# Performance work log

Measured on AMD Instinct MI355X. Metric: run time of the kernel, lower is better.

## Reference

```python
import jax, jax.numpy as jnp
import numpy as np


def setup_inputs() -> dict:
    key = jax.random.key(0)
    ks = jax.random.split(key, 13)
    B, T, I, H = 64, 512, 512, 1024
    s_in = 1.0 / np.sqrt(I)
    s_h = 1.0 / np.sqrt(H)
    d = {"x": jax.random.normal(ks[0], (B, T, I), jnp.float32)}
    names_U = ["U_i", "U_f", "U_c", "U_o"]
    names_V = ["V_i", "V_f", "V_c", "V_o"]
    names_b = ["b_i", "b_f", "b_c", "b_o"]
    for j in range(4):
        d[names_U[j]] = jax.random.normal(ks[1 + j], (I, H), jnp.float32) * s_in
        d[names_V[j]] = jax.random.normal(ks[5 + j], (H, H), jnp.float32) * s_h
        d[names_b[j]] = jax.random.normal(ks[9 + j], (H,), jnp.float32) * 0.01
    return d


def _lstm(x, U_i, V_i, b_i, U_f, V_f, b_f, U_c, V_c, b_c, U_o, V_o, b_o):
    B, T, I = x.shape
    H = U_i.shape[1]
    # Precompute input projections for all gates across time: [T, B, 4H]
    U = jnp.concatenate([U_i, U_f, U_c, U_o], axis=1)      # [I, 4H]
    V = jnp.concatenate([V_i, V_f, V_c, V_o], axis=1)      # [H, 4H]
    b = jnp.concatenate([b_i, b_f, b_c, b_o], axis=0)      # [4H]
    xU = jnp.einsum('bti,ig->tbg', x, U) + b               # [T, B, 4H]

    h0 = jnp.zeros((B, H), x.dtype)
    c0 = jnp.zeros((B, H), x.dtype)

    def step(carry, xu_t):
        h, c = carry
        gates = xu_t + h @ V                               # [B, 4H]
        i_t = jax.nn.sigmoid(gates[:, 0 * H:1 * H])
        f_t = jax.nn.sigmoid(gates[:, 1 * H:2 * H])
        g_t = jnp.tanh(gates[:, 2 * H:3 * H])
        o_t = jax.nn.sigmoid(gates[:, 3 * H:4 * H])
        c_new = f_t * c + i_t * g_t
        h_new = o_t * jnp.tanh(c_new)
        return (h_new, c_new), h_new

    (h_T, c_T), hs = jax.lax.scan(step, (h0, c0), xU)      # hs: [T, B, H]
    hidden_seq = jnp.transpose(hs, (1, 0, 2))              # [B, T, H]
    return hidden_seq, h_T, c_T


def reference(x, U_i, V_i, b_i, U_f, V_f, b_f, U_c, V_c, b_c, U_o, V_o, b_o):
    return _lstm(x, U_i, V_i, b_i, U_f, V_f, b_f, U_c, V_c, b_c, U_o, V_o, b_o)
```

## Files before the change

kernel.cpp:

```cpp
#include <hip/hip_runtime.h>

typedef __attribute__((ext_vector_type(8))) _Float16 f16x8;
typedef __attribute__((ext_vector_type(4))) _Float16 f16x4;
typedef __attribute__((ext_vector_type(4))) float f32x4;

#define B_SZ 64
#define T_SZ 512
#define I_SZ 512
#define H_SZ 1024
#define G4   4096
#define NBLK 256

__global__ void trans_kernel(const float* __restrict__ src, _Float16* __restrict__ dst,
                             int R, int q) {
  __shared__ float tile[64][65];
  const int n0 = blockIdx.x * 64;
  const int r0 = blockIdx.y * 64;
  const int x = threadIdx.x & 63, y = threadIdx.x >> 6;
  #pragma unroll
  for (int it = 0; it < 16; ++it) {
    int r = y * 16 + it;
    tile[r][x] = src[(size_t)(r0 + r) * H_SZ + n0 + x];
  }
  __syncthreads();
  #pragma unroll
  for (int it = 0; it < 16; ++it) {
    int rn = y * 16 + it;
    dst[(size_t)(4 * (n0 + rn) + q) * R + r0 + x] = (_Float16)tile[x][rn];
  }
}

__global__ void bias_kernel(const float* __restrict__ b0, const float* __restrict__ b1,
                            const float* __restrict__ b2, const float* __restrict__ b3,
                            float* __restrict__ dst) {
  int g = blockIdx.x * blockDim.x + threadIdx.x;
  if (g >= G4) return;
  int q = g & 3, n = g >> 2;
  const float* s = (q == 0) ? b0 : (q == 1) ? b1 : (q == 2) ? b2 : b3;
  dst[g] = s[n];
}

__device__ __forceinline__ unsigned short f2h(float f) {
  union { unsigned short s; _Float16 h; } c; c.h = (_Float16)f; return c.s;
}

__device__ __forceinline__ void x_issue(const float* x, int b0, int tid, int t, f32x4* xst) {
  #pragma unroll
  for (int j = 0; j < 8; ++j) {
    const int byteoff = j * 4096 + tid * 16;
    const int row  = byteoff >> 11;
    const int colb = byteoff & 2047;
    const char* sp = (const char*)x + (((size_t)(b0 + row) * T_SZ + t) * I_SZ) * 4 + colb;
    asm volatile("global_load_dwordx4 %0, %1, off" : "=v"(xst[j]) : "v"(sp) : "memory");
  }
}
__device__ __forceinline__ void x_write(char* xl, int tid, const f32x4* xst) {
  #pragma unroll
  for (int j = 0; j < 8; ++j) {
    const int byteoff = j * 4096 + tid * 16;
    const int row  = byteoff >> 11;
    const int colb = (byteoff & 2047) >> 1;
    f16x4 v = { (_Float16)xst[j].x, (_Float16)xst[j].y,
                (_Float16)xst[j].z, (_Float16)xst[j].w };
    *(f16x4*)(xl + (row << 10) + (colb ^ ((row & 7) << 4))) = v;
  }
}

__global__ __launch_bounds__(256, 1) void lstm_recur(
    const float* __restrict__ x,
    const _Float16* __restrict__ Ubt,
    const _Float16* __restrict__ Vt,
    const float* __restrict__ biasw,
    float* __restrict__ out,
    _Float16* __restrict__ hbuf,
    unsigned* __restrict__ bar)
{
  __shared__ __align__(16) char hsh[32768];
  __shared__ __align__(16) char xlds[32768];

  const int tid  = threadIdx.x;
  const int wv   = tid >> 6;
  const int lane = tid & 63;
  const int lc   = lane & 15;
  const int lk   = lane >> 4;
  const int blk  = blockIdx.x;
  const int bgrp = blk & 3;
  const int hgrp = blk >> 2;
  const int col0 = hgrp * 64 + wv * 16;
  const int b0   = bgrp * 16;
  const int sw   = (lc & 7) << 4;

  unsigned* flags = bar + bgrp * 256;

  f16x8 bU[16];
  f16x8 bV[32];
  {
    const _Float16* up = Ubt + (size_t)(col0 + lc) * I_SZ + lk * 8;
    #pragma unroll
    for (int ks = 0; ks < 16; ++ks) bU[ks] = *(const f16x8*)(up + ks * 32);
    const _Float16* vp = Vt + (size_t)(col0 + lc) * H_SZ + lk * 8;
    #pragma unroll
    for (int ks = 0; ks < 32; ++ks) bV[ks] = *(const f16x8*)(vp + ks * 32);
  }
  #pragma unroll
  for (int ks = 0; ks < 16; ++ks) asm volatile("" : "+v"(bU[ks]));
  #pragma unroll
  for (int ks = 0; ks < 32; ++ks) asm volatile("" : "+v"(bV[ks]));

  const f32x4 bias4 = *(const f32x4*)(biasw + col0 + lk * 4);
  const int n_gl = hgrp * 16 + wv * 4 + lk;
  const int brow = b0 + lc;
  const size_t HO = (size_t)B_SZ * T_SZ * H_SZ;
  const size_t CO = HO + (size_t)B_SZ * H_SZ;

  float cst = 0.f;

  const int grow = tid >> 4;
  const int gkb  = (tid & 15) * 16;
  const int gsw  = (grow & 7) << 4;

  f32x4 xst[8];
  x_issue(x, b0, tid, 0, xst);
  asm volatile("s_waitcnt vmcnt(0)" ::: "memory");
  __builtin_amdgcn_sched_barrier(0);
  x_write(xlds, tid, xst);
  asm volatile("s_waitcnt lgkmcnt(0)" ::: "memory");
  __builtin_amdgcn_s_barrier();
  __builtin_amdgcn_sched_barrier(0);

#define XPROJ(ks) { \
    const f16x8 a_ = *(const f16x8*)(xl_cur + (lc << 10) + ((((ks) * 64) + lk * 16) ^ sw)); \
    acc[(ks) & 3] = __builtin_amdgcn_mfma_f32_16x16x32_f16(bU[(ks)], a_, acc[(ks) & 3], 0, 0, 0); }
#define HPROJ(ks) { \
    const f16x8 hv = *(const f16x8*)(hsh + (lc << 11) + (((lk * 16) + (ks) * 64) ^ sw)); \
    acc[(ks) & 3] = __builtin_amdgcn_mfma_f32_16x16x32_f16(bV[(ks)], hv, acc[(ks) & 3], 0, 0, 0); }

  for (int t = 0; t < T_SZ; ++t) {
    const _Float16* hcur  = hbuf + (size_t)(t & 1) * (B_SZ * H_SZ);
    _Float16*       hnext = hbuf + (size_t)((t + 1) & 1) * (B_SZ * H_SZ);
    char* xl_cur = xlds + (size_t)(t & 1) * 16384;
    char* xl_nxt = xlds + (size_t)((t + 1) & 1) * 16384;

    if (t + 1 < T_SZ) x_issue(x, b0, tid, t + 1, xst);

    f32x4 acc[4];
    acc[0] = bias4;
    acc[1] = f32x4{0.f, 0.f, 0.f, 0.f};
    acc[2] = f32x4{0.f, 0.f, 0.f, 0.f};
    acc[3] = f32x4{0.f, 0.f, 0.f, 0.f};

    #pragma unroll
    for (int ks = 0; ks < 16; ++ks) XPROJ(ks);

    if (t) {
      if (wv == 0) {
        const unsigned* fp = flags + lane;
        unsigned v;
        do {
          asm volatile("global_load_dword %0, %1, off sc0 sc1\n\ts_waitcnt vmcnt(0)"
                       : "=&v"(v) : "v"(fp) : "memory");
        } while (__any(v < (unsigned)t));
      }
      __builtin_amdgcn_s_barrier();
      __builtin_amdgcn_sched_barrier(0);
    }

    f16x8 st0, st1, st2, st3, st4, st5, st6, st7;
    {
      const char* src = (const char*)(hcur + (size_t)b0 * H_SZ) + grow * 2048 + gkb;
      asm volatile("global_load_dwordx4 %0, %1, off sc0 sc1" : "=v"(st0) : "v"(src)          : "memory");
      asm volatile("global_load_dwordx4 %0, %1, off sc0 sc1" : "=v"(st1) : "v"(src + 256)    : "memory");
      asm volatile("global_load_dwordx4 %0, %1, off sc0 sc1" : "=v"(st2) : "v"(src + 512)    : "memory");
      asm volatile("global_load_dwordx4 %0, %1, off sc0 sc1" : "=v"(st3) : "v"(src + 768)    : "memory");
      asm volatile("global_load_dwordx4 %0, %1, off sc0 sc1" : "=v"(st4) : "v"(src + 1024)   : "memory");
      asm volatile("global_load_dwordx4 %0, %1, off sc0 sc1" : "=v"(st5) : "v"(src + 1280)   : "memory");
      asm volatile("global_load_dwordx4 %0, %1, off sc0 sc1" : "=v"(st6) : "v"(src + 1536)   : "memory");
      asm volatile("global_load_dwordx4 %0, %1, off sc0 sc1" : "=v"(st7) : "v"(src + 1792)   : "memory");
    }

    asm volatile("s_waitcnt vmcnt(4)" ::: "memory");
    __builtin_amdgcn_sched_barrier(0);
    *(f16x8*)(hsh + (grow << 11) + ((gkb +   0) ^ gsw)) = st0;
    *(f16x8*)(hsh + (grow << 11) + ((gkb + 256) ^ gsw)) = st1;
    *(f16x8*)(hsh + (grow << 11) + ((gkb + 512) ^ gsw)) = st2;
    *(f16x8*)(hsh + (grow << 11) + ((gkb + 768) ^ gsw)) = st3;
    asm volatile("s_waitcnt lgkmcnt(0)" ::: "memory");
    __builtin_amdgcn_s_barrier();
    __builtin_amdgcn_sched_barrier(0);

    #pragma unroll
    for (int ks = 0; ks < 16; ++ks) HPROJ(ks);

    asm volatile("s_waitcnt vmcnt(0)" ::: "memory");
    __builtin_amdgcn_sched_barrier(0);
    *(f16x8*)(hsh + (grow << 11) + ((gkb + 1024) ^ gsw)) = st4;
    *(f16x8*)(hsh + (grow << 11) + ((gkb + 1280) ^ gsw)) = st5;
    *(f16x8*)(hsh + (grow << 11) + ((gkb + 1536) ^ gsw)) = st6;
    *(f16x8*)(hsh + (grow << 11) + ((gkb + 1792) ^ gsw)) = st7;
    if (t + 1 < T_SZ) x_write(xl_nxt, tid, xst);
    asm volatile("s_waitcnt lgkmcnt(0)" ::: "memory");
    __builtin_amdgcn_s_barrier();
    __builtin_amdgcn_sched_barrier(0);

    #pragma unroll
    for (int ks = 16; ks < 32; ++ks) HPROJ(ks);

    const float vi = acc[0][0] + acc[1][0] + acc[2][0] + acc[3][0];
    const float vf = acc[0][1] + acc[1][1] + acc[2][1] + acc[3][1];
    const float vg = acc[0][2] + acc[1][2] + acc[2][2] + acc[3][2];
    const float vo = acc[0][3] + acc[1][3] + acc[2][3] + acc[3][3];
    const float gi = 1.f / (1.f + __expf(-vi));
    const float gf = 1.f / (1.f + __expf(-vf));
    const float sg = 1.f / (1.f + __expf(-2.f * vg));
    const float gg = 2.f * sg - 1.f;
    const float go = 1.f / (1.f + __expf(-vo));
    const float cn = gf * cst + gi * gg;
    const float sc2 = 1.f / (1.f + __expf(-2.f * cn));
    const float hn = go * (2.f * sc2 - 1.f);
    cst = cn;

    if (t < T_SZ - 1) {
      const unsigned short hv16 = f2h(hn);
      _Float16* hp2 = hnext + (size_t)brow * H_SZ + n_gl;
      asm volatile("global_store_short %0, %1, off sc0 sc1" :: "v"(hp2), "v"(hv16) : "memory");
    }
    asm volatile("s_waitcnt vmcnt(0)" ::: "memory");
    __builtin_amdgcn_s_barrier();
    if (t < T_SZ - 1 && tid == 64) {
      const unsigned* fp = flags + hgrp;
      unsigned tv = (unsigned)(t + 1);
      asm volatile("global_store_dword %0, %1, off sc0 sc1" :: "v"(fp), "v"(tv) : "memory");
    }

    out[(size_t)brow * (T_SZ * H_SZ) + (size_t)t * H_SZ + n_gl] = hn;
    if (t == T_SZ - 1) {
      out[HO + (size_t)brow * H_SZ + n_gl] = hn;
      out[CO + (size_t)brow * H_SZ + n_gl] = cn;
    }
  }
#undef XPROJ
#undef HPROJ
}

extern "C" void kernel_launch(void* const* d_in, const int* in_sizes, int n_in,
                              void* d_out, int out_size, void* d_ws, size_t ws_size,
                              hipStream_t stream) {
  const float* x = (const float*)d_in[0];
  const float* U[4]  = {(const float*)d_in[1], (const float*)d_in[4],
                        (const float*)d_in[7], (const float*)d_in[10]};
  const float* V[4]  = {(const float*)d_in[2], (const float*)d_in[5],
                        (const float*)d_in[8], (const float*)d_in[11]};
  const float* bb[4] = {(const float*)d_in[3], (const float*)d_in[6],
                        (const float*)d_in[9], (const float*)d_in[12]};
  float* out = (float*)d_out;

  char* p = (char*)d_ws;
  _Float16* Ubt = (_Float16*)p; p += (size_t)G4 * I_SZ * 2;
  _Float16* Vt  = (_Float16*)p; p += (size_t)G4 * H_SZ * 2;
  float*    biasw = (float*)p;  p += (size_t)G4 * 4;
  _Float16* hbuf  = (_Float16*)p; p += (size_t)2 * B_SZ * H_SZ * 2;
  unsigned* bar   = (unsigned*)p;

  for (int qq = 0; qq < 4; ++qq)
    hipLaunchKernelGGL(trans_kernel, dim3(16, 8), dim3(256), 0, stream, U[qq], Ubt, I_SZ, qq);
  for (int qq = 0; qq < 4; ++qq)
    hipLaunchKernelGGL(trans_kernel, dim3(16, 16), dim3(256), 0, stream, V[qq], Vt, H_SZ, qq);
  hipLaunchKernelGGL(bias_kernel, dim3(16), dim3(256), 0, stream, bb[0], bb[1], bb[2], bb[3], biasw);

  hipMemsetAsync(hbuf, 0, (size_t)B_SZ * H_SZ * 2, stream);
  hipMemsetAsync(bar, 0, 16384, stream);

  hipLaunchKernelGGL(lstm_recur, dim3(NBLK), dim3(256), 0, stream,
                     x, Ubt, Vt, biasw, out, hbuf, bar);
}
```

Before: 1.867 ms.

## Split K across waves, load h directly into registers, reduce partials via LDS

Each wave now covers a quarter of the K dimension for all 64 block columns instead of all of K for 16 columns. Each lane reads its h fragment straight from global memory into registers, so the h staging through shared memory and one barrier go away. MFMAs are issued as each h load arrives. The four per-wave partial sums are then combined through a small LDS buffer before the gate math. In exchange, every wave waits on all its global loads before the reduction, and the LDS partial-sum pass is new work.

After: 1.762 ms. 1.06x faster.

```diff
diff --git a/kernel.cpp b/kernel.cpp
--- a/kernel.cpp
+++ b/kernel.cpp
@@ -75,8 +75,8 @@
     _Float16* __restrict__ hbuf,
     unsigned* __restrict__ bar)
 {
-  __shared__ __align__(16) char hsh[32768];
   __shared__ __align__(16) char xlds[32768];
+  __shared__ __align__(16) float pbuf[4][16][68];
 
   const int tid  = threadIdx.x;
   const int wv   = tid >> 6;
@@ -86,7 +86,6 @@
   const int blk  = blockIdx.x;
   const int bgrp = blk & 3;
   const int hgrp = blk >> 2;
-  const int col0 = hgrp * 64 + wv * 16;
   const int b0   = bgrp * 16;
   const int sw   = (lc & 7) << 4;
 
@@ -94,30 +93,29 @@
 
   f16x8 bU[16];
   f16x8 bV[32];
-  {
-    const _Float16* up = Ubt + (size_t)(col0 + lc) * I_SZ + lk * 8;
-    #pragma unroll
-    for (int ks = 0; ks < 16; ++ks) bU[ks] = *(const f16x8*)(up + ks * 32);
-    const _Float16* vp = Vt + (size_t)(col0 + lc) * H_SZ + lk * 8;
-    #pragma unroll
-    for (int ks = 0; ks < 32; ++ks) bV[ks] = *(const f16x8*)(vp + ks * 32);
+  #pragma unroll
+  for (int ct = 0; ct < 4; ++ct) {
+    const int colg = hgrp * 64 + ct * 16 + lc;
+    const _Float16* up = Ubt + (size_t)colg * I_SZ + wv * 128 + lk * 8;
+    #pragma unroll
+    for (int ks = 0; ks < 4; ++ks) bU[ct * 4 + ks] = *(const f16x8*)(up + ks * 32);
+    const _Float16* vp = Vt + (size_t)colg * H_SZ + wv * 256 + lk * 8;
+    #pragma unroll
+    for (int ks = 0; ks < 8; ++ks) bV[ct * 8 + ks] = *(const f16x8*)(vp + ks * 32);
   }
   #pragma unroll
   for (int ks = 0; ks < 16; ++ks) asm volatile("" : "+v"(bU[ks]));
   #pragma unroll
   for (int ks = 0; ks < 32; ++ks) asm volatile("" : "+v"(bV[ks]));
 
-  const f32x4 bias4 = *(const f32x4*)(biasw + col0 + lk * 4);
-  const int n_gl = hgrp * 16 + wv * 4 + lk;
-  const int brow = b0 + lc;
+  const int nl    = wv * 4 + lk;
+  const int n_gl  = hgrp * 16 + nl;
+  const int brow  = b0 + lc;
+  const f32x4 bias4 = *(const f32x4*)(biasw + hgrp * 64 + nl * 4);
   const size_t HO = (size_t)B_SZ * T_SZ * H_SZ;
   const size_t CO = HO + (size_t)B_SZ * H_SZ;
 
   float cst = 0.f;
-
-  const int grow = tid >> 4;
-  const int gkb  = (tid & 15) * 16;
-  const int gsw  = (grow & 7) << 4;
 
   f32x4 xst[8];
   x_issue(x, b0, tid, 0, xst);
@@ -128,12 +126,11 @@
   __builtin_amdgcn_s_barrier();
   __builtin_amdgcn_sched_barrier(0);
 
-#define XPROJ(ks) { \
-    const f16x8 a_ = *(const f16x8*)(xl_cur + (lc << 10) + ((((ks) * 64) + lk * 16) ^ sw)); \
-    acc[(ks) & 3] = __builtin_amdgcn_mfma_f32_16x16x32_f16(bU[(ks)], a_, acc[(ks) & 3], 0, 0, 0); }
-#define HPROJ(ks) { \
-    const f16x8 hv = *(const f16x8*)(hsh + (lc << 11) + (((lk * 16) + (ks) * 64) ^ sw)); \
-    acc[(ks) & 3] = __builtin_amdgcn_mfma_f32_16x16x32_f16(bV[(ks)], hv, acc[(ks) & 3], 0, 0, 0); }
+#define HSTEP(ks, hv) { \
+    acc[0] = __builtin_amdgcn_mfma_f32_16x16x32_f16(bV[0 * 8 + (ks)], hv, acc[0], 0, 0, 0); \
+    acc[1] = __builtin_amdgcn_mfma_f32_16x16x32_f16(bV[1 * 8 + (ks)], hv, acc[1], 0, 0, 0); \
+    acc[2] = __builtin_amdgcn_mfma_f32_16x16x32_f16(bV[2 * 8 + (ks)], hv, acc[2], 0, 0, 0); \
+    acc[3] = __builtin_amdgcn_mfma_f32_16x16x32_f16(bV[3 * 8 + (ks)], hv, acc[3], 0, 0, 0); }
 
   for (int t = 0; t < T_SZ; ++t) {
     const _Float16* hcur  = hbuf + (size_t)(t & 1) * (B_SZ * H_SZ);
@@ -144,13 +141,20 @@
     if (t + 1 < T_SZ) x_issue(x, b0, tid, t + 1, xst);
 
     f32x4 acc[4];
-    acc[0] = bias4;
+    acc[0] = f32x4{0.f, 0.f, 0.f, 0.f};
     acc[1] = f32x4{0.f, 0.f, 0.f, 0.f};
     acc[2] = f32x4{0.f, 0.f, 0.f, 0.f};
     acc[3] = f32x4{0.f, 0.f, 0.f, 0.f};
 
     #pragma unroll
-    for (int ks = 0; ks < 16; ++ks) XPROJ(ks);
+    for (int ks = 0; ks < 4; ++ks) {
+      const f16x8 xa = *(const f16x8*)(xl_cur + (lc << 10) +
+                                       ((wv * 256 + ks * 64 + lk * 16) ^ sw));
+      acc[0] = __builtin_amdgcn_mfma_f32_16x16x32_f16(bU[0 * 4 + ks], xa, acc[0], 0, 0, 0);
+      acc[1] = __builtin_amdgcn_mfma_f32_16x16x32_f16(bU[1 * 4 + ks], xa, acc[1], 0, 0, 0);
+      acc[2] = __builtin_amdgcn_mfma_f32_16x16x32_f16(bU[2 * 4 + ks], xa, acc[2], 0, 0, 0);
+      acc[3] = __builtin_amdgcn_mfma_f32_16x16x32_f16(bU[3 * 4 + ks], xa, acc[3], 0, 0, 0);
+    }
 
     if (t) {
       if (wv == 0) {
@@ -165,55 +169,59 @@
       __builtin_amdgcn_sched_barrier(0);
     }
 
-    f16x8 st0, st1, st2, st3, st4, st5, st6, st7;
+    asm volatile("s_waitcnt vmcnt(0)" ::: "memory");
+    __builtin_amdgcn_sched_barrier(0);
+
+    f16x8 hv0, hv1, hv2, hv3, hv4, hv5, hv6, hv7;
     {
-      const char* src = (const char*)(hcur + (size_t)b0 * H_SZ) + grow * 2048 + gkb;
-      asm volatile("global_load_dwordx4 %0, %1, off sc0 sc1" : "=v"(st0) : "v"(src)          : "memory");
-      asm volatile("global_load_dwordx4 %0, %1, off sc0 sc1" : "=v"(st1) : "v"(src + 256)    : "memory");
-      asm volatile("global_load_dwordx4 %0, %1, off sc0 sc1" : "=v"(st2) : "v"(src + 512)    : "memory");
-      asm volatile("global_load_dwordx4 %0, %1, off sc0 sc1" : "=v"(st3) : "v"(src + 768)    : "memory");
-      asm volatile("global_load_dwordx4 %0, %1, off sc0 sc1" : "=v"(st4) : "v"(src + 1024)   : "memory");
-      asm volatile("global_load_dwordx4 %0, %1, off sc0 sc1" : "=v"(st5) : "v"(src + 1280)   : "memory");
-      asm volatile("global_load_dwordx4 %0, %1, off sc0 sc1" : "=v"(st6) : "v"(src + 1536)   : "memory");
-      asm volatile("global_load_dwordx4 %0, %1, off sc0 sc1" : "=v"(st7) : "v"(src + 1792)   : "memory");
-    }
-
-    asm volatile("s_waitcnt vmcnt(4)" ::: "memory");
-    __builtin_amdgcn_sched_barrier(0);
-    *(f16x8*)(hsh + (grow << 11) + ((gkb +   0) ^ gsw)) = st0;
-    *(f16x8*)(hsh + (grow << 11) + ((gkb + 256) ^ gsw)) = st1;
-    *(f16x8*)(hsh + (grow << 11) + ((gkb + 512) ^ gsw)) = st2;
-    *(f16x8*)(hsh + (grow << 11) + ((gkb + 768) ^ gsw)) = st3;
+      const char* hp = (const char*)hcur + (size_t)brow * 2048 + wv * 512 + lk * 16;
+      asm volatile("global_load_dwordx4 %0, %1, off sc0 sc1" : "=v"(hv0) : "v"(hp)        : "memory");
+      asm volatile("global_load_dwordx4 %0, %1, off sc0 sc1" : "=v"(hv1) : "v"(hp + 64)   : "memory");
+      asm volatile("global_load_dwordx4 %0, %1, off sc0 sc1" : "=v"(hv2) : "v"(hp + 128)  : "memory");
+      asm volatile("global_load_dwordx4 %0, %1, off sc0 sc1" : "=v"(hv3) : "v"(hp + 192)  : "memory");
+      asm volatile("global_load_dwordx4 %0, %1, off sc0 sc1" : "=v"(hv4) : "v"(hp + 256)  : "memory");
+      asm volatile("global_load_dwordx4 %0, %1, off sc0 sc1" : "=v"(hv5) : "v"(hp + 320)  : "memory");
+      asm volatile("global_load_dwordx4 %0, %1, off sc0 sc1" : "=v"(hv6) : "v"(hp + 384)  : "memory");
+      asm volatile("global_load_dwordx4 %0, %1, off sc0 sc1" : "=v"(hv7) : "v"(hp + 448)  : "memory");
+    }
+
+    if (t + 1 < T_SZ) x_write(xl_nxt, tid, xst);
+
+    asm volatile("s_waitcnt vmcnt(7)" ::: "memory"); __builtin_amdgcn_sched_barrier(0);
+    HSTEP(0, hv0);
+    asm volatile("s_waitcnt vmcnt(6)" ::: "memory"); __builtin_amdgcn_sched_barrier(0);
+    HSTEP(1, hv1);
+    asm volatile("s_waitcnt vmcnt(5)" ::: "memory"); __builtin_amdgcn_sched_barrier(0);
+    HSTEP(2, hv2);
+    asm volatile("s_waitcnt vmcnt(4)" ::: "memory"); __builtin_amdgcn_sched_barrier(0);
+    HSTEP(3, hv3);
+    asm volatile("s_waitcnt vmcnt(3)" ::: "memory"); __builtin_amdgcn_sched_barrier(0);
+    HSTEP(4, hv4);
+    asm volatile("s_waitcnt vmcnt(2)" ::: "memory"); __builtin_amdgcn_sched_barrier(0);
+    HSTEP(5, hv5);
+    asm volatile("s_waitcnt vmcnt(1)" ::: "memory"); __builtin_amdgcn_sched_barrier(0);
+    HSTEP(6, hv6);
+    asm volatile("s_waitcnt vmcnt(0)" ::: "memory"); __builtin_amdgcn_sched_barrier(0);
+    HSTEP(7, hv7);
+
+    #pragma unroll
+    for (int ct = 0; ct < 4; ++ct)
+      *(f32x4*)&pbuf[wv][lc][ct * 16 + lk * 4] = acc[ct];
     asm volatile("s_waitcnt lgkmcnt(0)" ::: "memory");
     __builtin_amdgcn_s_barrier();
     __builtin_amdgcn_sched_barrier(0);
 
-    #pragma unroll
-    for (int ks = 0; ks < 16; ++ks) HPROJ(ks);
-
-    asm volatile("s_waitcnt vmcnt(0)" ::: "memory");
-    __builtin_amdgcn_sched_barrier(0);
-    *(f16x8*)(hsh + (grow << 11) + ((gkb + 1024) ^ gsw)) = st4;
-    *(f16x8*)(hsh + (grow << 11) + ((gkb + 1280) ^ gsw)) = st5;
-    *(f16x8*)(hsh + (grow << 11) + ((gkb + 1536) ^ gsw)) = st6;
-    *(f16x8*)(hsh + (grow << 11) + ((gkb + 1792) ^ gsw)) = st7;
-    if (t + 1 < T_SZ) x_write(xl_nxt, tid, xst);
-    asm volatile("s_waitcnt lgkmcnt(0)" ::: "memory");
-    __builtin_amdgcn_s_barrier();
-    __builtin_amdgcn_sched_barrier(0);
-
-    #pragma unroll
-    for (int ks = 16; ks < 32; ++ks) HPROJ(ks);
-
-    const float vi = acc[0][0] + acc[1][0] + acc[2][0] + acc[3][0];
-    const float vf = acc[0][1] + acc[1][1] + acc[2][1] + acc[3][1];
-    const float vg = acc[0][2] + acc[1][2] + acc[2][2] + acc[3][2];
-    const float vo = acc[0][3] + acc[1][3] + acc[2][3] + acc[3][3];
-    const float gi = 1.f / (1.f + __expf(-vi));
-    const float gf = 1.f / (1.f + __expf(-vf));
-    const float sg = 1.f / (1.f + __expf(-2.f * vg));
+    f32x4 s = bias4;
+    #pragma unroll
+    for (int w = 0; w < 4; ++w) {
+      const f32x4 pv = *(const f32x4*)&pbuf[w][lc][nl * 4];
+      s.x += pv.x; s.y += pv.y; s.z += pv.z; s.w += pv.w;
+    }
+    const float gi = 1.f / (1.f + __expf(-s.x));
+    const float gf = 1.f / (1.f + __expf(-s.y));
+    const float sg = 1.f / (1.f + __expf(-2.f * s.z));
     const float gg = 2.f * sg - 1.f;
-    const float go = 1.f / (1.f + __expf(-vo));
+    const float go = 1.f / (1.f + __expf(-s.w));
     const float cn = gf * cst + gi * gg;
     const float sc2 = 1.f / (1.f + __expf(-2.f * cn));
     const float hn = go * (2.f * sc2 - 1.f);
@@ -238,8 +246,7 @@
       out[CO + (size_t)brow * H_SZ + n_gl] = cn;
     }
   }
-#undef XPROJ
-#undef HPROJ
+#undef HSTEP
 }
 
 extern "C" void kernel_launch(void* const* d_in, const int* in_sizes, int n_in,
```
